# Performance work log

Measured on AMD Instinct MI355X. Metric: run time of the kernel, lower is better.

Reference implementation:

```python
import jax, jax.numpy as jnp
import numpy as np
import math

B = 131072          # number of (user, item) pairs
NUM_USERS = 500000
NUM_ITEMS = 200000
HIDDEN = 512
BIN_SIZE = 0.5
MIN_RATING = 0.5
MAX_RATING = 5.0
NUM_BINS = int((MAX_RATING - MIN_RATING) / BIN_SIZE) + 1  # 10


def setup_inputs() -> dict:
    key = jax.random.key(0)
    k_uid, k_iid, k_uf, k_if = jax.random.split(key, 4)
    uid_input = jax.random.randint(k_uid, (B,), 0, NUM_USERS)
    iid_input = jax.random.randint(k_iid, (B,), 0, NUM_ITEMS)
    # Parameters, initialized exactly as init_initializers does for
    # thresholds_use_item=False (the default config):
    uid_features = jax.random.normal(k_uf, (NUM_USERS, HIDDEN), dtype=jnp.float32) * 0.01
    iid_features = jax.random.normal(k_if, (NUM_ITEMS, HIDDEN), dtype=jnp.float32) * 0.01
    uid_bias = jnp.zeros((NUM_USERS, 1), dtype=jnp.float32)
    iid_bias = jnp.full((NUM_ITEMS, 1), 3.5, dtype=jnp.float32)
    uid_t1 = jnp.full((NUM_USERS, 1), MIN_RATING + 0.5 * BIN_SIZE, dtype=jnp.float32)  # 0.75
    uid_beta = jnp.full((NUM_USERS, NUM_BINS - 2), math.log(BIN_SIZE), dtype=jnp.float32)
    return {
        "uid_input": uid_input,
        "iid_input": iid_input,
        "uid_features": uid_features,
        "iid_features": iid_features,
        "uid_bias": uid_bias,
        "iid_bias": iid_bias,
        "uid_t1": uid_t1,
        "uid_beta": uid_beta,
    }


def reference(uid_input, iid_input, uid_features, iid_features,
              uid_bias, iid_bias, uid_t1, uid_beta):
    # Multi-table gathers
    uf = uid_features[uid_input]          # [B, H]
    vf = iid_features[iid_input]          # [B, H]
    ub = uid_bias[uid_input]              # [B, 1]
    ib = iid_bias[iid_input]              # [B, 1]
    t1 = uid_t1[uid_input]                # [B, 1]
    beta = jnp.exp(uid_beta[uid_input])   # [B, NUM_BINS-2]

    # Score: u.v + item bias + user bias (default path: use_biases=True,
    # thresholds_use_item=False)
    uTi = jnp.sum(uf * vf, axis=-1, keepdims=True)   # [B, 1]
    y_ui = uTi + ib + ub                             # [B, 1]

    # Thresholds: t1 + cumulative sum of [0, beta...]
    zeros1 = jnp.zeros_like(t1)
    beta_cum = jnp.cumsum(jnp.concatenate([zeros1, beta], axis=-1), axis=-1)  # [B, NB-1]
    T = t1 + beta_cum                                                          # [B, NB-1]
    edges = jnp.concatenate([T, jnp.full_like(t1, jnp.inf)], axis=-1)          # [B, NB]

    # Ordinal sigmoid-difference masses
    sig = jax.nn.sigmoid(T - y_ui)                                             # [B, NB-1]
    cdf = jnp.concatenate([zeros1, sig, jnp.ones_like(t1)], axis=-1)           # [B, NB+1]
    bins_mass = cdf[:, 1:] - cdf[:, :-1]                                       # [B, NB]

    bin_values = MIN_RATING + BIN_SIZE * jnp.arange(NUM_BINS, dtype=bins_mass.dtype)
    bins_mean = jnp.sum(bins_mass * bin_values, axis=-1)                       # [B]
    bins_mode = MIN_RATING + jnp.argmax(bins_mass, axis=-1).astype(jnp.float32) * BIN_SIZE

    return bins_mass, bins_mean, bins_mode, edges
```

## Files before the change

kernel.cpp:

```cpp
#include <hip/hip_runtime.h>
#include <math.h>
#include <float.h>

#define HIDDEN 512
#define NUM_BINS 10
#define MIN_RATING 0.5f
#define BIN_SIZE 0.5f

__global__ __launch_bounds__(256) void ordrec_kernel(
    const int* __restrict__ uid_input,
    const int* __restrict__ iid_input,
    const float* __restrict__ uid_features,
    const float* __restrict__ iid_features,
    const float* __restrict__ uid_bias,
    const float* __restrict__ iid_bias,
    const float* __restrict__ uid_t1,
    const float* __restrict__ uid_beta,
    float* __restrict__ out,
    int n)
{
    const int wave_in_block = threadIdx.x >> 6;
    const int lane = threadIdx.x & 63;
    const int pair = blockIdx.x * 4 + wave_in_block;
    if (pair >= n) return;

    const int uid = uid_input[pair];
    const int iid = iid_input[pair];

    const float4* uf = (const float4*)(uid_features + (size_t)uid * HIDDEN);
    const float4* vf = (const float4*)(iid_features + (size_t)iid * HIDDEN);

    float4 a0 = uf[lane];
    float4 a1 = uf[lane + 64];
    float4 b0 = vf[lane];
    float4 b1 = vf[lane + 64];

    float dot = a0.x * b0.x + a0.y * b0.y + a0.z * b0.z + a0.w * b0.w
              + a1.x * b1.x + a1.y * b1.y + a1.z * b1.z + a1.w * b1.w;

    #pragma unroll
    for (int off = 32; off > 0; off >>= 1)
        dot += __shfl_xor(dot, off, 64);

    const float ub = uid_bias[uid];
    const float ib = iid_bias[iid];
    const float t1 = uid_t1[uid];
    const float y  = dot + ib + ub;

    float b = 0.0f;
    if (lane >= 1 && lane <= 8)
        b = uid_beta[(size_t)uid * (NUM_BINS - 2) + (lane - 1)];
    float e = expf(b);
    e = (lane >= 1 && lane <= 8) ? e : 0.0f;

    float p = e;
    #pragma unroll
    for (int off = 1; off <= 8; off <<= 1) {
        float t = __shfl_up(p, off, 64);
        if (lane >= off) p += t;
    }
    const float T = t1 + p;

    const float sig = 1.0f / (1.0f + expf(-(T - y)));

    float s_lo = __shfl_up(sig, 1, 64);
    if (lane == 0) s_lo = 0.0f;
    const float s_hi = (lane == 9) ? 1.0f : sig;
    const float mass = s_hi - s_lo;

    float c = (lane < NUM_BINS) ? mass * (MIN_RATING + BIN_SIZE * (float)lane) : 0.0f;
    #pragma unroll
    for (int off = 1; off <= 8; off <<= 1)
        c += __shfl_xor(c, off, 16);
    float bm = (lane < NUM_BINS) ? mass : -1.0e30f;
    int   bi = lane;
    #pragma unroll
    for (int off = 1; off <= 8; off <<= 1) {
        float om = __shfl_xor(bm, off, 16);
        int   oi = __shfl_xor(bi, off, 16);
        if (om > bm || (om == bm && oi < bi)) { bm = om; bi = oi; }
    }
    const float mode = MIN_RATING + BIN_SIZE * (float)bi;

    float* out_mass  = out;
    float* out_mean  = out + (size_t)n * NUM_BINS;
    float* out_edges = out_mean + 2 * (size_t)n;

    if (lane < NUM_BINS) {
        out_mass [(size_t)pair * NUM_BINS + lane] = mass;
        out_edges[(size_t)pair * NUM_BINS + lane] = (lane == 9) ? 1.0e30f : T;
    }
    if (lane < 2) {
        out_mean[(size_t)lane * n + pair] = (lane == 0) ? c : mode;
    }
}

extern "C" void kernel_launch(void* const* d_in, const int* in_sizes, int n_in,
                              void* d_out, int out_size, void* d_ws, size_t ws_size,
                              hipStream_t stream) {
    const int*   uid_input    = (const int*)d_in[0];
    const int*   iid_input    = (const int*)d_in[1];
    const float* uid_features = (const float*)d_in[2];
    const float* iid_features = (const float*)d_in[3];
    const float* uid_bias     = (const float*)d_in[4];
    const float* iid_bias     = (const float*)d_in[5];
    const float* uid_t1       = (const float*)d_in[6];
    const float* uid_beta     = (const float*)d_in[7];
    float* out = (float*)d_out;

    const int n = in_sizes[0];
    const int blocks = (n + 3) / 4;

    ordrec_kernel<<<blocks, 256, 0, stream>>>(
        uid_input, iid_input, uid_features, iid_features,
        uid_bias, iid_bias, uid_t1, uid_beta, out, n);
}
```

Before: 100.1 us.

## Bucket pairs by item id so item-row gathers reuse cache

Adds two pre-kernels that clear a workspace and then scatter each pair index into one of 256 buckets keyed on item id, using atomic counters and an overflow region. The main kernel then walks the pairs in bucket order through a permutation, so pairs sharing a nearby item range run close together and reuse the item-feature rows in L2/MALL. This costs two extra launches, atomics, a workspace pass, and some empty slots in the main grid. Bucket capacity (768 per bucket plus 4096 overflow) depends on item ids being roughly uniform, and any pairs beyond that capacity are silently dropped.

```diff
diff --git a/kernel.cpp b/kernel.cpp
--- a/kernel.cpp
+++ b/kernel.cpp
@@ -7,6 +7,36 @@
 #define MIN_RATING 0.5f
 #define BIN_SIZE 0.5f
 
+#define NB   256
+#define CAP  768
+#define OVF  4096
+#define NSLOT (NB * CAP)
+#define SLOTS_OFF (NB + 1)
+#define WS_WORDS  (SLOTS_OFF + NSLOT + OVF)
+
+__global__ __launch_bounds__(256) void init_ws(unsigned int* __restrict__ ws) {
+    const int idx = blockIdx.x * 256 + threadIdx.x;
+    if (idx < SLOTS_OFF) ws[idx] = 0u;
+    if (idx < NSLOT + OVF) ws[SLOTS_OFF + idx] = 0xFFFFFFFFu;
+}
+
+__global__ __launch_bounds__(256) void scatter_pairs(
+    const int* __restrict__ iid_input, unsigned int* __restrict__ ws,
+    int n, int num_items)
+{
+    const int pair = blockIdx.x * 256 + threadIdx.x;
+    if (pair >= n) return;
+    const unsigned int iid = (unsigned int)iid_input[pair];
+    unsigned int b = (unsigned int)(((unsigned long long)iid * NB) / (unsigned int)num_items);
+    if (b >= NB) b = NB - 1;
+    const unsigned int slot = atomicAdd(&ws[b], 1u);
+    unsigned int s;
+    if (slot < CAP) s = b * CAP + slot;
+    else            s = NSLOT + atomicAdd(&ws[NB], 1u);
+    if (s < NSLOT + OVF) ws[SLOTS_OFF + s] = (unsigned int)pair;
+}
+
+template <bool USE_PERM>
 __global__ __launch_bounds__(256) void ordrec_kernel(
     const int* __restrict__ uid_input,
     const int* __restrict__ iid_input,
@@ -16,13 +46,23 @@
     const float* __restrict__ iid_bias,
     const float* __restrict__ uid_t1,
     const float* __restrict__ uid_beta,
+    const unsigned int* __restrict__ perm,
     float* __restrict__ out,
     int n)
 {
     const int wave_in_block = threadIdx.x >> 6;
     const int lane = threadIdx.x & 63;
-    const int pair = blockIdx.x * 4 + wave_in_block;
-    if (pair >= n) return;
+    const int slot = blockIdx.x * 4 + wave_in_block;
+
+    int pair;
+    if (USE_PERM) {
+        const unsigned int p = perm[slot];
+        if (p == 0xFFFFFFFFu) return;
+        pair = (int)p;
+    } else {
+        pair = slot;
+        if (pair >= n) return;
+    }
 
     const int uid = uid_input[pair];
     const int iid = iid_input[pair];
@@ -109,9 +149,22 @@
     float* out = (float*)d_out;
 
     const int n = in_sizes[0];
-    const int blocks = (n + 3) / 4;
+    const int num_items = in_sizes[3] / HIDDEN;
 
-    ordrec_kernel<<<blocks, 256, 0, stream>>>(
-        uid_input, iid_input, uid_features, iid_features,
-        uid_bias, iid_bias, uid_t1, uid_beta, out, n);
+    if (ws_size >= (size_t)WS_WORDS * 4) {
+        unsigned int* ws = (unsigned int*)d_ws;
+        const int init_blocks = (NSLOT + OVF + 255) / 256;
+        init_ws<<<init_blocks, 256, 0, stream>>>(ws);
+        scatter_pairs<<<(n + 255) / 256, 256, 0, stream>>>(iid_input, ws, n, num_items);
+        const int main_blocks = (NSLOT + OVF) / 4;
+        ordrec_kernel<true><<<main_blocks, 256, 0, stream>>>(
+            uid_input, iid_input, uid_features, iid_features,
+            uid_bias, iid_bias, uid_t1, uid_beta,
+            ws + SLOTS_OFF, out, n);
+    } else {
+        ordrec_kernel<false><<<(n + 3) / 4, 256, 0, stream>>>(
+            uid_input, iid_input, uid_features, iid_features,
+            uid_bias, iid_bias, uid_t1, uid_beta,
+            nullptr, out, n);
+    }
 }
```

Result: slower. 179.2 us (+79.0%).
